# Kernel tuning notes

Measured on AMD Instinct MI355X. Metric: run time of the kernel, lower is better.

## Reference

```python
import jax, jax.numpy as jnp
import numpy as np

B, T, C = 2, 2048, 2048
N_HEAD, N_GROUPS, HEAD_SIZE = 16, 4, 128
Q_PER_KV = N_HEAD // N_GROUPS  # 4
N_ELEM = HEAD_SIZE  # rotary_percentage = 1.0
HIDDEN = 4 * C
EPS = 1e-5


def layernorm(x, w, b):
    m = jnp.mean(x, axis=-1, keepdims=True)
    v = jnp.mean(jnp.square(x - m), axis=-1, keepdims=True)
    return (x - m) * jax.lax.rsqrt(v + EPS) * w + b


def apply_rope(x, cos, sin):
    # x: [B, H, T, n_elem]; cos/sin: [T, n_elem] (broadcast over B, H)
    d = x.shape[-1]
    x1, x2 = x[..., : d // 2], x[..., d // 2 :]
    rotated = jnp.concatenate((-x2, x1), axis=-1)
    return x * cos + rotated * sin


def setup_inputs() -> dict:
    key = jax.random.key(0)
    ks = jax.random.split(key, 8)
    x = jax.random.normal(ks[0], (B, T, C), dtype=jnp.float32)
    # rope cache (NeoX/LLaMA half-rotation layout), base 10000
    theta = 1.0 / (10000.0 ** (jnp.arange(0, N_ELEM, 2, dtype=jnp.float32) / N_ELEM))
    idx_theta = jnp.outer(jnp.arange(T, dtype=jnp.float32), theta)  # [T, n_elem//2]
    idx_theta = jnp.concatenate((idx_theta, idx_theta), axis=-1)    # [T, n_elem]
    cos, sin = jnp.cos(idx_theta), jnp.sin(idx_theta)
    mask = jnp.tril(jnp.ones((T, T), dtype=bool))[None, None]  # causal [1,1,T,T]
    s = 0.02
    return {
        "x": x,
        "cos": cos,
        "sin": sin,
        "ln1_w": jnp.ones((C,), jnp.float32),
        "ln1_b": jnp.zeros((C,), jnp.float32),
        "ln2_w": jnp.ones((C,), jnp.float32),
        "ln2_b": jnp.zeros((C,), jnp.float32),
        "w_attn": jax.random.normal(ks[1], (C, (N_HEAD + 2 * N_GROUPS) * HEAD_SIZE), jnp.float32) * s,
        "w_proj": jax.random.normal(ks[2], (C, C), jnp.float32) * s,
        "w_fc": jax.random.normal(ks[3], (C, HIDDEN), jnp.float32) * s,
        "w_mlp_proj": jax.random.normal(ks[4], (HIDDEN, C), jnp.float32) * s,
        "mask": mask,
    }


def reference(x, cos, sin, ln1_w, ln1_b, ln2_w, ln2_b, w_attn, w_proj, w_fc, w_mlp_proj, mask):
    n1 = layernorm(x, ln1_w, ln1_b)
    # fused QKV projection
    qkv = n1 @ w_attn  # [B, T, (H + 2G) * hs]
    qkv = qkv.reshape(B, T, N_GROUPS, Q_PER_KV + 2, HEAD_SIZE)
    q = qkv[:, :, :, :Q_PER_KV]      # [B, T, G, qpk, hs]
    k = qkv[:, :, :, Q_PER_KV]       # [B, T, G, hs]
    v = qkv[:, :, :, Q_PER_KV + 1]   # [B, T, G, hs]
    # q -> [B, H, T, hs] (group-major head order)
    q = q.transpose(0, 2, 3, 1, 4).reshape(B, N_HEAD, T, HEAD_SIZE)
    # k, v -> [B, G, T, hs] then repeat_interleave groups to H heads
    k = jnp.repeat(k.transpose(0, 2, 1, 3), Q_PER_KV, axis=1)  # [B, H, T, hs]
    v = jnp.repeat(v.transpose(0, 2, 1, 3), Q_PER_KV, axis=1)
    # RoPE on the first N_ELEM dims (here full head)
    q = jnp.concatenate((apply_rope(q[..., :N_ELEM], cos, sin), q[..., N_ELEM:]), axis=-1)
    k = jnp.concatenate((apply_rope(k[..., :N_ELEM], cos, sin), k[..., N_ELEM:]), axis=-1)
    scale = 1.0 / np.sqrt(HEAD_SIZE).astype(np.float32)
    att = jnp.einsum("bhtd,bhsd->bhts", q, k) * scale
    att = jnp.where(mask, att, jnp.finfo(att.dtype).min)
    att = jax.nn.softmax(att, axis=-1)
    y = jnp.einsum("bhts,bhsd->bhtd", att, v)
    y = y.transpose(0, 2, 1, 3).reshape(B, T, C)
    h = y @ w_proj
    # non-parallel residual (LLaMA-style): x + attn, then x + mlp(norm2(x))
    x = x + h
    n2 = layernorm(x, ln2_w, ln2_b)
    mlp = jax.nn.gelu(n2 @ w_fc, approximate=False) @ w_mlp_proj
    return x + mlp
```

## Files before the change

kernel.cpp:

```cpp
#include <hip/hip_runtime.h>
#include <stdint.h>
#include <math.h>

#define Tn   2048
#define Cn   2048
#define BTn  4096
#define NQKV 3072
#define HID  8192

typedef unsigned short u16;
typedef float f32x4 __attribute__((ext_vector_type(4)));
typedef short s16x8 __attribute__((ext_vector_type(8)));

__device__ __forceinline__ float b2f(u16 u) { return __uint_as_float(((unsigned)u) << 16); }
__device__ __forceinline__ u16 f2b(float f) {
  unsigned i = __float_as_uint(f);
  return (u16)((i + 0x7fffu + ((i >> 16) & 1u)) >> 16);
}

__device__ __forceinline__ void g2l16(const void* g, void* l) {
  __builtin_amdgcn_global_load_lds((const __attribute__((address_space(1))) unsigned int*)g,
                                   (__attribute__((address_space(3))) unsigned int*)l,
                                   16, 0, 0);
}

__global__ __launch_bounds__(256) void transpose_f2b(const float* __restrict__ in,
                                                     u16* __restrict__ out, int R, int C) {
  __shared__ float tile[32][33];
  int bx = blockIdx.x * 32, by = blockIdx.y * 32;
  int tx = threadIdx.x, ty = threadIdx.y;
  #pragma unroll
  for (int j = 0; j < 32; j += 8)
    tile[ty + j][tx] = in[(size_t)(by + ty + j) * C + bx + tx];
  __syncthreads();
  #pragma unroll
  for (int j = 0; j < 32; j += 8)
    out[(size_t)(bx + ty + j) * R + by + tx] = f2b(tile[tx][ty + j]);
}

__global__ __launch_bounds__(256) void transpose_u16(const u16* __restrict__ in,
                                                     u16* __restrict__ out, int R, int C) {
  __shared__ u16 tile[32][33];
  const size_t zb = (size_t)blockIdx.z * R * C;
  int bx = blockIdx.x * 32, by = blockIdx.y * 32;
  int tx = threadIdx.x, ty = threadIdx.y;
  #pragma unroll
  for (int j = 0; j < 32; j += 8)
    tile[ty + j][tx] = in[zb + (size_t)(by + ty + j) * C + bx + tx];
  __syncthreads();
  #pragma unroll
  for (int j = 0; j < 32; j += 8)
    out[zb + (size_t)(bx + ty + j) * R + by + tx] = tile[tx][ty + j];
}

__global__ __launch_bounds__(256)
void layernorm_k(const float* __restrict__ x, const float* __restrict__ w,
                 const float* __restrict__ bb, u16* __restrict__ out) {
  __shared__ float red[256];
  __shared__ float sm, sv;
  const int tid = threadIdx.x;
  const long row = blockIdx.x;
  const float* xr = x + row * (long)Cn;
  float v[8];
  float s = 0.f;
  #pragma unroll
  for (int i = 0; i < 8; ++i) { v[i] = xr[i * 256 + tid]; s += v[i]; }
  red[tid] = s; __syncthreads();
  for (int st = 128; st > 0; st >>= 1) { if (tid < st) red[tid] += red[tid + st]; __syncthreads(); }
  if (tid == 0) sm = red[0] * (1.f / Cn);
  __syncthreads();
  const float mean = sm;
  float s2 = 0.f;
  #pragma unroll
  for (int i = 0; i < 8; ++i) { float d = v[i] - mean; s2 += d * d; }
  red[tid] = s2; __syncthreads();
  for (int st = 128; st > 0; st >>= 1) { if (tid < st) red[tid] += red[tid + st]; __syncthreads(); }
  if (tid == 0) sv = rsqrtf(red[0] * (1.f / Cn) + 1e-5f);
  __syncthreads();
  const float rstd = sv;
  #pragma unroll
  for (int i = 0; i < 8; ++i) {
    int c = i * 256 + tid;
    out[row * (long)Cn + c] = f2b((v[i] - mean) * rstd * w[c] + bb[c]);
  }
}

__global__ __launch_bounds__(256)
void rope_split(const u16* __restrict__ qkv, const float* __restrict__ cs,
                const float* __restrict__ sn, u16* __restrict__ q,
                u16* __restrict__ k, u16* __restrict__ v) {
  const long idx = (long)blockIdx.x * 256 + threadIdx.x;
  const int row = (int)(idx / NQKV);
  const int col = (int)(idx % NQKV);
  const int b = row >> 11, t = row & 2047;
  const int g = col / 768, rr = col % 768, s = rr >> 7, d = rr & 127;
  const u16 raw = qkv[idx];
  if (s == 5) { v[((long)(b * 4 + g) * Tn + t) * 128 + d] = raw; return; }
  const float xv = b2f(raw);
  const float x2 = b2f(qkv[idx - d + (d ^ 64)]);
  const float c = cs[t * 128 + d];
  const float si = sn[t * 128 + d];
  const float rot = (d < 64) ? -x2 : x2;
  const float o = xv * c + rot * si;
  if (s == 4) k[((long)(b * 4 + g) * Tn + t) * 128 + d] = f2b(o);
  else        q[((long)(b * 16 + g * 4 + s) * Tn + t) * 128 + d] = f2b(o);
}

__global__ __launch_bounds__(256, 2)
void attn_flash(const u16* __restrict__ q, const u16* __restrict__ k,
                const u16* __restrict__ vt, u16* __restrict__ y) {
  __shared__ __align__(16) u16 Ks[4 * 64 * 32];
  __shared__ __align__(16) u16 Vs[2 * 128 * 32];
  __shared__ __align__(16) u16 Ps[4][2 * 16 * 32];
  const int tid = threadIdx.x, wave = tid >> 6, lane = tid & 63;
  const int fr = lane & 15, quad = lane >> 4;
  const int lr4 = lane >> 2, lc8 = (lane & 3) << 3;
  const int bx = blockIdx.x, bh = blockIdx.y;
  const int b = bh >> 4, h = bh & 15, g = h >> 2;
  const int bg = b * 4 + g;
  const u16* kg = k + (size_t)bg * Tn * 128;
  const u16* vg = vt + (size_t)bg * 128 * Tn;
  const int q0 = bx * 64 + wave * 16;

  s16x8 qf[4];
  {
    const u16* qrow = q + ((size_t)bh * Tn + q0 + fr) * 128;
    #pragma unroll
    for (int kc = 0; kc < 4; ++kc)
      qf[kc] = *(const s16x8*)(qrow + kc * 32 + quad * 8);
  }
  f32x4 o_acc[8] = {};
  float m_r[4], l_r[4];
  #pragma unroll
  for (int r = 0; r < 4; ++r) { m_r[r] = -1e30f; l_r[r] = 0.f; }
  const float scale = 0.08838834764831845f;

  for (int step = 0; step <= bx; ++step) {
    const int j0 = step * 64;
    __syncthreads();
    #pragma unroll
    for (int kc = 0; kc < 4; ++kc)
      g2l16(kg + (size_t)(j0 + wave * 16 + lr4) * 128 + kc * 32 + lc8,
            Ks + kc * 2048 + wave * 16 * 32);
    #pragma unroll
    for (int kc = 0; kc < 2; ++kc)
      #pragma unroll
      for (int hh = 0; hh < 2; ++hh)
        g2l16(vg + (size_t)(wave * 32 + hh * 16 + lr4) * Tn + j0 + kc * 32 + lc8,
              Vs + kc * 4096 + (wave * 32 + hh * 16) * 32);
    __syncthreads();

    f32x4 s[4] = {};
    #pragma unroll
    for (int kc = 0; kc < 4; ++kc)
      #pragma unroll
      for (int nt = 0; nt < 4; ++nt) {
        s16x8 bf = *(const s16x8*)(Ks + kc * 2048 + (nt * 16 + fr) * 32 + quad * 8);
        s[nt] = __builtin_amdgcn_mfma_f32_16x16x32_bf16(qf[kc], bf, s[nt], 0, 0, 0);
      }

    const bool diag = (step == bx);
    #pragma unroll
    for (int r = 0; r < 4; ++r) {
      float vmax = -1e30f;
      #pragma unroll
      for (int nt = 0; nt < 4; ++nt) {
        float sv = s[nt][r] * scale;
        if (diag && (j0 + nt * 16 + fr) > (q0 + quad * 4 + r)) sv = -1e30f;
        s[nt][r] = sv;
        vmax = fmaxf(vmax, sv);
      }
      #pragma unroll
      for (int mk = 1; mk < 16; mk <<= 1) vmax = fmaxf(vmax, __shfl_xor(vmax, mk, 64));
      const float mnew = fmaxf(m_r[r], vmax);
      const float alpha = __expf(m_r[r] - mnew);
      float rsum = 0.f;
      #pragma unroll
      for (int nt = 0; nt < 4; ++nt) {
        float pv = __expf(s[nt][r] - mnew);
        s[nt][r] = pv; rsum += pv;
      }
      #pragma unroll
      for (int mk = 1; mk < 16; mk <<= 1) rsum += __shfl_xor(rsum, mk, 64);
      l_r[r] = l_r[r] * alpha + rsum;
      m_r[r] = mnew;
      #pragma unroll
      for (int nt = 0; nt < 8; ++nt) o_acc[nt][r] *= alpha;
    }

    u16* pw = Ps[wave];
    #pragma unroll
    for (int nt = 0; nt < 4; ++nt) {
      const int col = nt * 16 + fr, pan = col >> 5, cc = col & 31;
      #pragma unroll
      for (int r = 0; r < 4; ++r)
        pw[pan * 512 + (quad * 4 + r) * 32 + cc] = f2b(s[nt][r]);
    }
    #pragma unroll
    for (int kc = 0; kc < 2; ++kc) {
      s16x8 af = *(const s16x8*)(pw + kc * 512 + fr * 32 + quad * 8);
      #pragma unroll
      for (int nt = 0; nt < 8; ++nt) {
        s16x8 bf = *(const s16x8*)(Vs + kc * 4096 + (nt * 16 + fr) * 32 + quad * 8);
        o_acc[nt] = __builtin_amdgcn_mfma_f32_16x16x32_bf16(af, bf, o_acc[nt], 0, 0, 0);
      }
    }
  }

  #pragma unroll
  for (int r = 0; r < 4; ++r) {
    const float inv = 1.f / l_r[r];
    const size_t row = (size_t)(b * Tn + q0 + quad * 4 + r) * Cn + h * 128;
    #pragma unroll
    for (int nt = 0; nt < 8; ++nt)
      y[row + nt * 16 + fr] = f2b(o_acc[nt][r] * inv);
  }
}

#define BAR  __builtin_amdgcn_s_barrier()
#define LG0  asm volatile("s_waitcnt lgkmcnt(0)" ::: "memory")
#define RD_A(BUF, MI4)                                                                  \
  { _Pragma("unroll") for (int m_ = 0; m_ < 4; ++m_) {                                  \
      _Pragma("unroll") for (int k_ = 0; k_ < 2; ++k_)                                  \
        ar[m_][k_] = *(const s16x8*)(Sb + (BUF) * 32768 + aBase +                       \
                                     (((MI4) + m_) << 11) + (k_ << 10) + fragoff); } }
#define RD_B(BUF, NI2, DST)                                                             \
  { _Pragma("unroll") for (int n_ = 0; n_ < 2; ++n_) {                                  \
      _Pragma("unroll") for (int k_ = 0; k_ < 2; ++k_)                                  \
        DST[n_][k_] = *(const s16x8*)(Sb + (BUF) * 32768 + bBase +                      \
                                      (((NI2) + n_) << 11) + (k_ << 10) + fragoff); } }
#define MM(MB, NB, BR)                                                                  \
  { __builtin_amdgcn_s_setprio(1);                                                     \
    _Pragma("unroll") for (int m_ = 0; m_ < 4; ++m_) {                                  \
      _Pragma("unroll") for (int n_ = 0; n_ < 2; ++n_) {                                \
        _Pragma("unroll") for (int k_ = 0; k_ < 2; ++k_)                                \
          acc[(MB) + m_][(NB) + n_] = __builtin_amdgcn_mfma_f32_16x16x32_bf16(          \
              ar[m_][k_], BR[n_][k_], acc[(MB) + m_][(NB) + n_], 0, 0, 0); } }          \
    __builtin_amdgcn_s_setprio(0); }

template <int EPI>
__global__ __launch_bounds__(512, 2)
void gemm256(const u16* __restrict__ A, const u16* __restrict__ Bt,
             const float* __restrict__ res, u16* __restrict__ ob,
             float* __restrict__ of, int M, int N, int K, int num_n) {
  __shared__ __align__(16) u16 S[65536];
  char* Sb = (char*)S;
  (void)M;

  const int pid = blockIdx.x;
  const int xcd = pid & 7, idx = pid >> 3;
  const int jj = idx & 3;
  const int gp = (idx >> 2) * 8 + xcd;
  const int npc = num_n >> 1;
  const int pr = gp / npc, pc = gp - pr * npc;
  const long m0 = (long)(pr * 2 + (jj >> 1)) * 256;
  const long n0 = (long)(pc * 2 + (jj & 1)) * 256;

  const int tid = (int)threadIdx.x;
  const int wave = tid >> 6, lane = tid & 63;
  const int wr = wave >> 2, wc = wave & 3;
  const int fr = lane & 15, quad = lane >> 4;
  const int fragoff = (fr * 64 + quad * 16) ^ (((fr >> 3) & 1) << 5);
  const int aBase = wr * 16384;
  const int bBase = 65536 + (wc >> 1) * 16384 + ((wc & 1) << 13);

  int srow[2], skcb[2];
  #pragma unroll
  for (int rr = 0; rr < 2; ++rr) {
    const int d = rr * 8192 + wave * 1024 + lane * 16;
    const int l = d ^ (((d >> 9) & 1) << 5);
    srow[rr] = ((l >> 11) << 4) | ((l >> 6) & 15);
    skcb[rr] = (((l >> 10) & 1) << 6) | (l & 63);
  }
  auto stage = [&](const u16* __restrict__ src, long grow0, int kt, int regionByte) {
    #pragma unroll
    for (int rr = 0; rr < 2; ++rr)
      g2l16((const char*)src + (grow0 + srow[rr]) * (long)K * 2 + (long)kt * 128 + skcb[rr],
            Sb + regionByte + rr * 8192 + wave * 1024);
  };

  const int nk = K >> 6;
  const int nk2 = nk >> 1;

  stage(A,  m0,       0, 0);
  stage(A,  m0 + 128, 0, 16384);
  stage(Bt, n0,       0, 65536);
  stage(Bt, n0 + 128, 0, 81920);
  stage(Bt, n0,       1, 98304);
  stage(Bt, n0 + 128, 1, 114688);
  asm volatile("s_waitcnt vmcnt(4)" ::: "memory");
  BAR;

  s16x8 ar[4][2], br0[2][2], br1[2][2];
  f32x4 acc[8][4] = {};

  for (int i = 0; i < nk2; ++i) {
    const int t1 = 2 * i + 1, s0 = 2 * i + 2, s1 = 2 * i + 3;
    const bool v0 = (s0 < nk), v1 = (s1 < nk);
    RD_A(0, 0); RD_B(0, 0, br0);
    stage(A, m0, t1, 32768);
    asm volatile("s_waitcnt lgkmcnt(8)" ::: "memory");
    BAR; LG0; MM(0, 0, br0); BAR;
    RD_B(0, 2, br1);
    stage(A, m0 + 128, t1, 49152);
    BAR; LG0; MM(0, 2, br1); BAR;
    RD_A(0, 4);
    if (v0) stage(Bt, n0, s0, 65536);
    BAR; LG0; MM(4, 2, br1); BAR;
    if (v0) stage(Bt, n0 + 128, s0, 81920);
    BAR; LG0; MM(4, 0, br0);
    if (v0) { asm volatile("s_waitcnt vmcnt(4)" ::: "memory"); }
    else    { asm volatile("s_waitcnt vmcnt(0)" ::: "memory"); }
    BAR;
    RD_A(1, 0); RD_B(1, 0, br0);
    if (v0) stage(A, m0, s0, 0);
    asm volatile("s_waitcnt lgkmcnt(8)" ::: "memory");
    BAR; LG0; MM(0, 0, br0); BAR;
    RD_B(1, 2, br1);
    if (v0) stage(A, m0 + 128, s0, 16384);
    BAR; LG0; MM(0, 2, br1); BAR;
    RD_A(1, 4);
    if (v1) stage(Bt, n0, s1, 98304);
    BAR; LG0; MM(4, 2, br1); BAR;
    if (v1) stage(Bt, n0 + 128, s1, 114688);
    BAR; LG0; MM(4, 0, br0);
    asm volatile("s_waitcnt vmcnt(4)" ::: "memory");
    BAR;
  }

  #pragma unroll
  for (int mi = 0; mi < 8; ++mi)
    #pragma unroll
    for (int ni = 0; ni < 4; ++ni)
      #pragma unroll
      for (int r = 0; r < 4; ++r) {
        const long row = m0 + wr * 128 + mi * 16 + quad * 4 + r;
        const long col = n0 + wc * 64 + ni * 16 + fr;
        const long idx2 = row * N + col;
        const float vv = acc[mi][ni][r];
        if (EPI == 0) ob[idx2] = f2b(vv);
        else if (EPI == 1) of[idx2] = vv + res[idx2];
        else ob[idx2] = f2b(0.5f * vv * (1.0f + erff(vv * 0.70710678118654752f)));
      }
}

extern "C" void kernel_launch(void* const* d_in, const int* in_sizes, int n_in,
                              void* d_out, int out_size, void* d_ws, size_t ws_size,
                              hipStream_t stream) {
  (void)in_sizes; (void)n_in; (void)out_size; (void)ws_size;
  const float* x      = (const float*)d_in[0];
  const float* cosb   = (const float*)d_in[1];
  const float* sinb   = (const float*)d_in[2];
  const float* ln1w   = (const float*)d_in[3];
  const float* ln1b   = (const float*)d_in[4];
  const float* ln2w   = (const float*)d_in[5];
  const float* ln2b   = (const float*)d_in[6];
  const float* w_attn = (const float*)d_in[7];
  const float* w_proj = (const float*)d_in[8];
  const float* w_fc   = (const float*)d_in[9];
  const float* w_mp   = (const float*)d_in[10];
  float* out = (float*)d_out;

  char* p = (char*)d_ws;
  auto alloc = [&](size_t bytes) { char* r = p; p += (bytes + 255) & ~(size_t)255; return (void*)r; };
  u16*  wT_attn = (u16*)alloc((size_t)NQKV * Cn * 2);
  u16*  wT_proj = (u16*)alloc((size_t)Cn * Cn * 2);
  u16*  wT_fc   = (u16*)alloc((size_t)HID * Cn * 2);
  u16*  wT_mp   = (u16*)alloc((size_t)Cn * HID * 2);
  u16*  n12     = (u16*)alloc((size_t)BTn * Cn * 2);
  u16*  qkv     = (u16*)alloc((size_t)BTn * NQKV * 2);
  u16*  qb      = (u16*)alloc((size_t)2 * 16 * Tn * 128 * 2);
  u16*  kb      = (u16*)alloc((size_t)2 * 4 * Tn * 128 * 2);
  u16*  vb      = (u16*)alloc((size_t)2 * 4 * Tn * 128 * 2);
  float* x1     = (float*)alloc((size_t)BTn * Cn * 4);
  u16*  hbuf    = (u16*)alloc((size_t)BTn * HID * 2);
  u16*  vt      = n12;

  dim3 tb(32, 8);
  transpose_f2b<<<dim3(NQKV / 32, Cn / 32), tb, 0, stream>>>(w_attn, wT_attn, Cn, NQKV);
  transpose_f2b<<<dim3(Cn / 32, Cn / 32), tb, 0, stream>>>(w_proj, wT_proj, Cn, Cn);
  transpose_f2b<<<dim3(HID / 32, Cn / 32), tb, 0, stream>>>(w_fc, wT_fc, Cn, HID);
  transpose_f2b<<<dim3(Cn / 32, HID / 32), tb, 0, stream>>>(w_mp, wT_mp, HID, Cn);

  layernorm_k<<<BTn, 256, 0, stream>>>(x, ln1w, ln1b, n12);
  gemm256<0><<<(BTn / 256) * (NQKV / 256), 512, 0, stream>>>(n12, wT_attn, nullptr, qkv, nullptr, BTn, NQKV, Cn, NQKV / 256);
  rope_split<<<(int)(((long)BTn * NQKV) / 256), 256, 0, stream>>>(qkv, cosb, sinb, qb, kb, vb);
  transpose_u16<<<dim3(128 / 32, Tn / 32, 8), tb, 0, stream>>>(vb, vt, Tn, 128);
  attn_flash<<<dim3(Tn / 64, 32), 256, 0, stream>>>(qb, kb, vt, qkv );
  gemm256<1><<<(BTn / 256) * (Cn / 256), 512, 0, stream>>>(qkv, wT_proj, x, nullptr, x1, BTn, Cn, Cn, Cn / 256);
  layernorm_k<<<BTn, 256, 0, stream>>>(x1, ln2w, ln2b, n12);
  gemm256<2><<<(BTn / 256) * (HID / 256), 512, 0, stream>>>(n12, wT_fc, nullptr, hbuf, nullptr, BTn, HID, Cn, HID / 256);
  gemm256<1><<<(BTn / 256) * (Cn / 256), 512, 0, stream>>>(hbuf, wT_mp, x1, nullptr, out, BTn, Cn, HID, Cn / 256);
}
```

Measured before the change: 908.4 us.

## Split-K the two residual GEMMs with atomic accumulation and trim GEMM barriers

The attention projection and MLP down-projection GEMMs now split K in two across a second grid dimension, and each half atomically adds its partial sums into an output pre-filled with the residual by a new copy kernel. Only 128 tiles existed for these N=2048 GEMMs, so splitting doubles block count to fill more CUs. It also removes several barriers and the lgkmcnt waits inside the main GEMM loop for all GEMMs. Costs are extra residual copy passes, fp32 atomic traffic, nondeterministic summation order, and a possible LDS read race from the removed waits and barriers.

```diff
diff --git a/kernel.cpp b/kernel.cpp
--- a/kernel.cpp
+++ b/kernel.cpp
@@ -51,6 +51,12 @@
   #pragma unroll
   for (int j = 0; j < 32; j += 8)
     out[zb + (size_t)(bx + ty + j) * R + by + tx] = tile[tx][ty + j];
+}
+
+__global__ __launch_bounds__(256)
+void copy_f32(const float* __restrict__ in, float* __restrict__ out) {
+  const long i = ((long)blockIdx.x * 256 + threadIdx.x) * 4;
+  *(f32x4*)(out + i) = *(const f32x4*)(in + i);
 }
 
 __global__ __launch_bounds__(256)
@@ -242,10 +248,12 @@
 __global__ __launch_bounds__(512, 2)
 void gemm256(const u16* __restrict__ A, const u16* __restrict__ Bt,
              const float* __restrict__ res, u16* __restrict__ ob,
-             float* __restrict__ of, int M, int N, int K, int num_n) {
+             float* __restrict__ of, int N, int Kl, int ld, int num_n) {
   __shared__ __align__(16) u16 S[65536];
   char* Sb = (char*)S;
-  (void)M;
+
+  const long koff = (long)blockIdx.y * Kl;
+  A += koff; Bt += koff;
 
   const int pid = blockIdx.x;
   const int xcd = pid & 7, idx = pid >> 3;
@@ -275,11 +283,11 @@
   auto stage = [&](const u16* __restrict__ src, long grow0, int kt, int regionByte) {
     #pragma unroll
     for (int rr = 0; rr < 2; ++rr)
-      g2l16((const char*)src + (grow0 + srow[rr]) * (long)K * 2 + (long)kt * 128 + skcb[rr],
+      g2l16((const char*)src + (grow0 + srow[rr]) * (long)ld * 2 + (long)kt * 128 + skcb[rr],
             Sb + regionByte + rr * 8192 + wave * 1024);
   };
 
-  const int nk = K >> 6;
+  const int nk = Kl >> 6;
   const int nk2 = nk >> 1;
 
   stage(A,  m0,       0, 0);
@@ -299,31 +307,29 @@
     const bool v0 = (s0 < nk), v1 = (s1 < nk);
     RD_A(0, 0); RD_B(0, 0, br0);
     stage(A, m0, t1, 32768);
-    asm volatile("s_waitcnt lgkmcnt(8)" ::: "memory");
-    BAR; LG0; MM(0, 0, br0); BAR;
+    LG0; MM(0, 0, br0); BAR;
     RD_B(0, 2, br1);
     stage(A, m0 + 128, t1, 49152);
-    BAR; LG0; MM(0, 2, br1); BAR;
+    LG0; MM(0, 2, br1); BAR;
     RD_A(0, 4);
     if (v0) stage(Bt, n0, s0, 65536);
-    BAR; LG0; MM(4, 2, br1); BAR;
+    LG0; MM(4, 2, br1); BAR;
     if (v0) stage(Bt, n0 + 128, s0, 81920);
-    BAR; LG0; MM(4, 0, br0);
+    MM(4, 0, br0);
     if (v0) { asm volatile("s_waitcnt vmcnt(4)" ::: "memory"); }
     else    { asm volatile("s_waitcnt vmcnt(0)" ::: "memory"); }
     BAR;
     RD_A(1, 0); RD_B(1, 0, br0);
     if (v0) stage(A, m0, s0, 0);
-    asm volatile("s_waitcnt lgkmcnt(8)" ::: "memory");
-    BAR; LG0; MM(0, 0, br0); BAR;
+    LG0; MM(0, 0, br0); BAR;
     RD_B(1, 2, br1);
     if (v0) stage(A, m0 + 128, s0, 16384);
-    BAR; LG0; MM(0, 2, br1); BAR;
+    LG0; MM(0, 2, br1); BAR;
     RD_A(1, 4);
     if (v1) stage(Bt, n0, s1, 98304);
-    BAR; LG0; MM(4, 2, br1); BAR;
+    LG0; MM(4, 2, br1); BAR;
     if (v1) stage(Bt, n0 + 128, s1, 114688);
-    BAR; LG0; MM(4, 0, br0);
+    MM(4, 0, br0);
     asm volatile("s_waitcnt vmcnt(4)" ::: "memory");
     BAR;
   }
@@ -340,7 +346,8 @@
         const float vv = acc[mi][ni][r];
         if (EPI == 0) ob[idx2] = f2b(vv);
         else if (EPI == 1) of[idx2] = vv + res[idx2];
-        else ob[idx2] = f2b(0.5f * vv * (1.0f + erff(vv * 0.70710678118654752f)));
+        else if (EPI == 2) ob[idx2] = f2b(0.5f * vv * (1.0f + erff(vv * 0.70710678118654752f)));
+        else atomicAdd(&of[idx2], vv);
       }
 }
 
@@ -383,12 +390,14 @@
   transpose_f2b<<<dim3(Cn / 32, HID / 32), tb, 0, stream>>>(w_mp, wT_mp, HID, Cn);
 
   layernorm_k<<<BTn, 256, 0, stream>>>(x, ln1w, ln1b, n12);
-  gemm256<0><<<(BTn / 256) * (NQKV / 256), 512, 0, stream>>>(n12, wT_attn, nullptr, qkv, nullptr, BTn, NQKV, Cn, NQKV / 256);
+  gemm256<0><<<(BTn / 256) * (NQKV / 256), 512, 0, stream>>>(n12, wT_attn, nullptr, qkv, nullptr, NQKV, Cn, Cn, NQKV / 256);
   rope_split<<<(int)(((long)BTn * NQKV) / 256), 256, 0, stream>>>(qkv, cosb, sinb, qb, kb, vb);
   transpose_u16<<<dim3(128 / 32, Tn / 32, 8), tb, 0, stream>>>(vb, vt, Tn, 128);
   attn_flash<<<dim3(Tn / 64, 32), 256, 0, stream>>>(qb, kb, vt, qkv );
-  gemm256<1><<<(BTn / 256) * (Cn / 256), 512, 0, stream>>>(qkv, wT_proj, x, nullptr, x1, BTn, Cn, Cn, Cn / 256);
+  copy_f32<<<(int)(((long)BTn * Cn) / 1024), 256, 0, stream>>>(x, x1);
+  gemm256<3><<<dim3((BTn / 256) * (Cn / 256), 2), 512, 0, stream>>>(qkv, wT_proj, nullptr, nullptr, x1, Cn, Cn / 2, Cn, Cn / 256);
   layernorm_k<<<BTn, 256, 0, stream>>>(x1, ln2w, ln2b, n12);
-  gemm256<2><<<(BTn / 256) * (HID / 256), 512, 0, stream>>>(n12, wT_fc, nullptr, hbuf, nullptr, BTn, HID, Cn, HID / 256);
-  gemm256<1><<<(BTn / 256) * (Cn / 256), 512, 0, stream>>>(hbuf, wT_mp, x1, nullptr, out, BTn, Cn, HID, Cn / 256);
-}
+  gemm256<2><<<(BTn / 256) * (HID / 256), 512, 0, stream>>>(n12, wT_fc, nullptr, hbuf, nullptr, HID, Cn, Cn, HID / 256);
+  copy_f32<<<(int)(((long)BTn * Cn) / 1024), 256, 0, stream>>>(x1, out);
+  gemm256<3><<<dim3((BTn / 256) * (Cn / 256), 2), 512, 0, stream>>>(hbuf, wT_mp, nullptr, nullptr, out, Cn, HID / 2, HID, Cn / 256);
+}
```

New measurement: 883.4 us. 2.7% less time.
